# Kernel optimization log

Measured on AMD Instinct MI355X. Metric: run time of the kernel, lower is better.

The kernel has to match this reference:

```python
import jax, jax.numpy as jnp
import numpy as np

HEADS = 16


def setup_inputs() -> dict:
    key = jax.random.key(0)
    ks = jax.random.split(key, 7)
    b, n, dim = 4, 1024, 1024
    s = 1.0 / np.sqrt(dim)
    return {
        "x": jax.random.normal(ks[0], (b, n, dim), dtype=jnp.float32),
        "Wq": jax.random.normal(ks[1], (dim, dim), dtype=jnp.float32) * s,
        "bq": jax.random.normal(ks[2], (dim,), dtype=jnp.float32) * 0.01,
        "Wv": jax.random.normal(ks[3], (dim, dim), dtype=jnp.float32) * s,
        "bv": jax.random.normal(ks[4], (dim,), dtype=jnp.float32) * 0.01,
        "Wo": jax.random.normal(ks[5], (dim, dim), dtype=jnp.float32) * s,
        "bo": jax.random.normal(ks[6], (dim,), dtype=jnp.float32) * 0.01,
    }


def reference(x, Wq, bq, Wv, bv, Wo, bo):
    b, n, dim = x.shape
    h = HEADS
    d = dim // h
    scale = d ** -0.5

    # projections (torch Linear: x @ W.T + b), split heads: b n (h d) -> b h n d
    q = (x @ Wq.T + bq).reshape(b, n, h, d).transpose(0, 2, 1, 3)
    v = (x @ Wv.T + bv).reshape(b, n, h, d).transpose(0, 2, 1, 3)

    # pairwise L2 distance scores: ||q_i||^2 - 2 q_i.q_j + ||q_j||^2
    dots = jnp.einsum("bhnd,bhmd->bhnm", q, q)          # [b,h,n,n]
    sq = jnp.sum(q * q, axis=-1)                          # [b,h,n]
    scores = -(sq[..., :, None] - 2.0 * dots + sq[..., None, :]) * scale
    attn = jax.nn.softmax(scores, axis=-1)

    out = jnp.einsum("bhnm,bhmd->bhnd", attn, v)          # [b,h,n,d]
    out = out.transpose(0, 2, 1, 3).reshape(b, n, dim)    # b h n d -> b n (h d)
    return out @ Wo.T + bo
```

## Files before the change

kernel.cpp:

```cpp
#include <hip/hip_runtime.h>
#include <hip/hip_bf16.h>

typedef __hip_bfloat16 bf16;
typedef short short8 __attribute__((ext_vector_type(8)));
typedef float floatx4 __attribute__((ext_vector_type(4)));
typedef unsigned uintx4 __attribute__((ext_vector_type(4)));
typedef unsigned short ushort;

#define MFMA __builtin_amdgcn_mfma_f32_16x16x32_bf16

#define BATCH 4
#define SEQ   1024
#define DIM   1024
#define HEADS 16
#define HD    64
#define RS    72


__device__ __forceinline__ float b2f(ushort u) {
    union { unsigned i; float f; } x; x.i = (unsigned)u << 16; return x.f;
}
__device__ __forceinline__ ushort f2b(float f) {
    union { float f; unsigned i; } x; x.f = f;
    return (ushort)((x.i + 0x7FFFu + ((x.i >> 16) & 1u)) >> 16);
}

__device__ __forceinline__ void nts16(void* p, uint4 v) {
    uintx4 x; x.x = v.x; x.y = v.y; x.z = v.z; x.w = v.w;
    __builtin_nontemporal_store(x, (uintx4*)p);
}
__device__ __forceinline__ void nts16f(void* p, float4 v) {
    floatx4 x; x.x = v.x; x.y = v.y; x.z = v.z; x.w = v.w;
    __builtin_nontemporal_store(x, (floatx4*)p);
}
__device__ __forceinline__ void nts2(ushort* p, ushort v) {
    __builtin_nontemporal_store(v, p);
}

__device__ __forceinline__ void gload16(const ushort* gp, ushort* lp) {
    __builtin_amdgcn_global_load_lds(
        (const __attribute__((address_space(1))) unsigned*)gp,
        (__attribute__((address_space(3))) unsigned*)lp, 16, 0, 0);
}

__device__ __forceinline__ short8 cvt8(uint4 a, uint4 b) {
    const float* f0 = (const float*)&a;
    const float* f1 = (const float*)&b;
    union { __hip_bfloat162 h; unsigned u; } c0, c1, c2, c3;
    float2 p;
    p.x = f0[0]; p.y = f0[1]; c0.h = __float22bfloat162_rn(p);
    p.x = f0[2]; p.y = f0[3]; c1.h = __float22bfloat162_rn(p);
    p.x = f1[0]; p.y = f1[1]; c2.h = __float22bfloat162_rn(p);
    p.x = f1[2]; p.y = f1[3]; c3.h = __float22bfloat162_rn(p);
    short8 s;
    unsigned* su = (unsigned*)&s;
    su[0] = c0.u; su[1] = c1.u; su[2] = c2.u; su[3] = c3.u;
    return s;
}

__global__ __launch_bounds__(256)
void conv_x(const float* __restrict__ x, ushort* __restrict__ xb)
{
    const size_t g = (size_t)blockIdx.x * 256 + threadIdx.x;
    const uint4* xv = (const uint4*)x;
    uint4 a = xv[g * 2], b = xv[g * 2 + 1];
    short8 s = cvt8(a, b);
    nts16(xb + g * 8, *(uint4*)&s);
}

template<int OUT>
__global__ __launch_bounds__(256, 3)
void gemm_core(const ushort* __restrict__ Ab,
               const float* __restrict__ W0, const float* __restrict__ b0,
               const float* __restrict__ W1, const float* __restrict__ b1,
               ushort* __restrict__ Qd, ushort* __restrict__ Vd,
               float* __restrict__ Fd)
{
    __shared__ __align__(16) ushort SMEM[2 * 128 * 64 + 64 * RS];
    ushort* A0  = SMEM;
    ushort* A1  = SMEM + 8192;
    ushort* Bsm = SMEM + 16384;

    const int t = threadIdx.x;
    const int w = t >> 6, lane = t & 63;
    const int lr = lane & 15, quad = lane >> 4;
    const int isV = (!OUT) && (blockIdx.x >= 16);
    const int n0 = (blockIdx.x & 15) * 64;
    const int m0 = blockIdx.y * 128;
    const float* __restrict__ W    = isV ? W1 : W0;
    const float* __restrict__ bias = isV ? b1 : b0;
    const int mw = (w >> 1) * 64, nw = (w & 1) * 32;
    const int ar = t >> 3, ac8 = (t & 7) * 8;

    const int arow = (lane >> 3);
    const int acS  = ((lane & 7) ^ arow) * 8;

    uint4 wpre[4];
    #pragma unroll
    for (int c = 0; c < 2; ++c) {
        const float* wp = W + (size_t)(n0 + c * 32 + ar) * DIM + ac8;
        wpre[2 * c]     = *(const uint4*)wp;
        wpre[2 * c + 1] = *(const uint4*)(wp + 4);
    }
    {
        #pragma unroll
        for (int i = 0; i < 4; ++i) {
            const int chunk = w * 4 + i;
            const int row = chunk * 8 + arow;
            gload16(Ab + (size_t)(m0 + row) * DIM + acS,
                    A0 + chunk * 512);
        }
    }

    floatx4 acc[4][2];
    const floatx4 fz = {0.f, 0.f, 0.f, 0.f};
    #pragma unroll
    for (int i = 0; i < 4; ++i)
        #pragma unroll
        for (int j = 0; j < 2; ++j) acc[i][j] = fz;

    ushort* Acur = A0;
    ushort* Anxt = A1;

    for (int kt = 0; kt < 16; ++kt) {
        #pragma unroll
        for (int c = 0; c < 2; ++c)
            *(short8*)&Bsm[(c * 32 + ar) * RS + ac8] = cvt8(wpre[2 * c], wpre[2 * c + 1]);
        __syncthreads();
        if (kt < 15) {
            const int k0 = (kt + 1) * 64;
            #pragma unroll
            for (int i = 0; i < 4; ++i) {
                const int chunk = w * 4 + i;
                const int row = chunk * 8 + arow;
                gload16(Ab + (size_t)(m0 + row) * DIM + k0 + acS,
                        Anxt + chunk * 512);
            }
            #pragma unroll
            for (int c = 0; c < 2; ++c) {
                const float* wp = W + (size_t)(n0 + c * 32 + ar) * DIM + k0 + ac8;
                wpre[2 * c]     = *(const uint4*)wp;
                wpre[2 * c + 1] = *(const uint4*)(wp + 4);
            }
        }
        #pragma unroll
        for (int ks = 0; ks < 2; ++ks) {
            short8 af[4], bfx[2];
            #pragma unroll
            for (int tm = 0; tm < 4; ++tm) {
                const int rowa = mw + tm * 16 + lr;
                const int csw  = ((ks * 4 + quad) ^ (lr & 7)) * 8;
                af[tm] = *(const short8*)&Acur[rowa * 64 + csw];
            }
            #pragma unroll
            for (int tn = 0; tn < 2; ++tn)
                bfx[tn] = *(const short8*)&Bsm[(nw + tn * 16 + lr) * RS + ks * 32 + quad * 8];
            #pragma unroll
            for (int tm = 0; tm < 4; ++tm)
                #pragma unroll
                for (int tn = 0; tn < 2; ++tn)
                    acc[tm][tn] = MFMA(af[tm], bfx[tn], acc[tm][tn], 0, 0, 0);
        }
        __syncthreads();
        ushort* tmp = Acur; Acur = Anxt; Anxt = tmp;
    }

    if (OUT) {
        float* TF = (float*)SMEM;
        #pragma unroll
        for (int pass = 0; pass < 2; ++pass) {
            __syncthreads();
            if ((w >> 1) == pass) {
                #pragma unroll
                for (int tn = 0; tn < 2; ++tn) {
                    const float bval = bias[n0 + nw + tn * 16 + lr];
                    #pragma unroll
                    for (int tm = 0; tm < 4; ++tm)
                        #pragma unroll
                        for (int r = 0; r < 4; ++r)
                            TF[(tm * 16 + quad * 4 + r) * 68 + nw + tn * 16 + lr] =
                                acc[tm][tn][r] + bval;
                }
            }
            __syncthreads();
            #pragma unroll
            for (int it = 0; it < 4; ++it) {
                const int cid = it * 256 + t;
                const int row = cid >> 4, c4 = (cid & 15) * 4;
                nts16f(Fd + (size_t)(m0 + pass * 64 + row) * DIM + n0 + c4,
                       *(const float4*)&TF[row * 68 + c4]);
            }
        }
        return;
    }

    const int bb = m0 >> 10, ii0 = m0 & 1023;
    const int head = blockIdx.x & 15;
    const int bh = bb * HEADS + head;
    if (!isV) {
        #pragma unroll
        for (int tn = 0; tn < 2; ++tn) {
            const float bval = bias[n0 + nw + tn * 16 + lr];
            #pragma unroll
            for (int tm = 0; tm < 4; ++tm)
                #pragma unroll
                for (int r = 0; r < 4; ++r)
                    SMEM[(mw + tm * 16 + quad * 4 + r) * 80 + nw + tn * 16 + lr] =
                        f2b(acc[tm][tn][r] + bval);
        }
        __syncthreads();
        #pragma unroll
        for (int it = 0; it < 4; ++it) {
            const int cid = it * 256 + t;
            const int row = cid >> 3, col8 = (cid & 7) * 8;
            nts16(Qd + ((size_t)bh * SEQ + ii0 + row) * HD + col8,
                  *(const uint4*)&SMEM[row * 80 + col8]);
        }
    } else {
        #pragma unroll
        for (int tn = 0; tn < 2; ++tn) {
            const float bval = bias[n0 + nw + tn * 16 + lr];
            #pragma unroll
            for (int tm = 0; tm < 4; ++tm)
                #pragma unroll
                for (int r = 0; r < 4; ++r)
                    SMEM[(nw + tn * 16 + lr) * 144 + mw + tm * 16 + quad * 4 + r] =
                        f2b(acc[tm][tn][r] + bval);
        }
        __syncthreads();
        #pragma unroll
        for (int it = 0; it < 4; ++it) {
            const int cid = it * 256 + t;
            const int row = cid >> 4, col8 = (cid & 15) * 8;
            nts16(Vd + ((size_t)bh * HD + row) * SEQ + ii0 + col8,
                  *(const uint4*)&SMEM[row * 144 + col8]);
        }
    }
}

__global__ __launch_bounds__(256)
void attn_mfma(const ushort* __restrict__ Q, const ushort* __restrict__ Vt,
               ushort* __restrict__ O)
{
    __shared__ __align__(16) ushort Ps[128 * RS];
    __shared__ __align__(16) ushort Ks[64 * RS];
    __shared__ __align__(16) ushort Vs[64 * RS];
    __shared__ float sqq[128], sqk[64];

    const int t = threadIdx.x;
    const int w = t >> 6, lane = t & 63;
    const int lr = lane & 15, quad = lane >> 4;
    const int id = blockIdx.x;
    const int bh = id & 63;
    const int i0 = (id >> 6) * 128;
    const ushort* __restrict__ Qp = Q  + (size_t)bh * SEQ * HD;
    const ushort* __restrict__ Vp = Vt + (size_t)bh * HD * SEQ;

    const int sr = t >> 3, sc8 = (t & 7) * 8;

    #pragma unroll
    for (int it = 0; it < 4; ++it) {
        const int cid = it * 256 + t;
        const int r = cid >> 3, c8 = (cid & 7) * 8;
        *(uint4*)&Ps[r * RS + c8] = *(const uint4*)(Qp + (size_t)(i0 + r) * HD + c8);
    }
    __syncthreads();

    {
        const int qsub = quad & 1, half = quad >> 1;
        const int qr = w * 32 + qsub * 16 + lr, ch = half * 32;
        float s = 0.f;
        #pragma unroll
        for (int cc = 0; cc < 4; ++cc) {
            uint4 k = *(const uint4*)&Ps[qr * RS + ch + cc * 8];
            const ushort* u = (const ushort*)&k;
            #pragma unroll
            for (int e = 0; e < 8; ++e) { float f = b2f(u[e]); s += f * f; }
        }
        s += __shfl_xor(s, 32);
        if (half == 0) sqq[qr] = s;
    }
    __syncthreads();

    short8 qa[2][2];
    #pragma unroll
    for (int tm = 0; tm < 2; ++tm)
        #pragma unroll
        for (int ks = 0; ks < 2; ++ks)
            qa[tm][ks] = *(const short8*)&Ps[(w * 32 + tm * 16 + lr) * RS + ks * 32 + quad * 8];
    float sqi[2][4];
    #pragma unroll
    for (int tm = 0; tm < 2; ++tm)
        #pragma unroll
        for (int r = 0; r < 4; ++r)
            sqi[tm][r] = sqq[w * 32 + tm * 16 + quad * 4 + r];

    floatx4 oacc[2][4];
    const floatx4 fz = {0.f, 0.f, 0.f, 0.f};
    float lrow[2][4] = {};
    #pragma unroll
    for (int tm = 0; tm < 2; ++tm)
        #pragma unroll
        for (int td = 0; td < 4; ++td) oacc[tm][td] = fz;

    for (int jt = 0; jt < 16; ++jt) {
        const int j0 = jt * 64;
        __syncthreads();
        #pragma unroll
        for (int it = 0; it < 2; ++it) {
            const int r = it * 32 + sr;
            *(uint4*)&Ks[r * RS + sc8] = *(const uint4*)(Qp + (size_t)(j0 + r) * HD + sc8);
            *(uint4*)&Vs[r * RS + sc8] = *(const uint4*)(Vp + (size_t)r * SEQ + j0 + sc8);
        }
        __syncthreads();

        {
            const int jr = w * 16 + lr, ch = quad * 16;
            uint4 k1 = *(const uint4*)&Ks[jr * RS + ch];
            uint4 k2 = *(const uint4*)&Ks[jr * RS + ch + 8];
            const ushort* u1 = (const ushort*)&k1;
            const ushort* u2 = (const ushort*)&k2;
            float s = 0.f;
            #pragma unroll
            for (int cc = 0; cc < 8; ++cc) {
                float f1 = b2f(u1[cc]), f2 = b2f(u2[cc]);
                s += f1 * f1 + f2 * f2;
            }
            s += __shfl_xor(s, 16);
            s += __shfl_xor(s, 32);
            if (quad == 0) sqk[jr] = s;
        }
        __syncthreads();

        float sq4[4];
        #pragma unroll
        for (int tn = 0; tn < 4; ++tn) sq4[tn] = sqk[tn * 16 + lr];

        short8 kb[4][2];
        #pragma unroll
        for (int tn = 0; tn < 4; ++tn)
            #pragma unroll
            for (int ks = 0; ks < 2; ++ks)
                kb[tn][ks] = *(const short8*)&Ks[(tn * 16 + lr) * RS + ks * 32 + quad * 8];

        #pragma unroll
        for (int tm = 0; tm < 2; ++tm) {
            floatx4 sacc[4];
            #pragma unroll
            for (int tn = 0; tn < 4; ++tn) {
                floatx4 a = MFMA(qa[tm][0], kb[tn][0], fz, 0, 0, 0);
                sacc[tn]  = MFMA(qa[tm][1], kb[tn][1], a, 0, 0, 0);
            }
            float sc[4][4];
            #pragma unroll
            for (int tn = 0; tn < 4; ++tn) {
                const float msq = -0.125f * sq4[tn];
                #pragma unroll
                for (int r = 0; r < 4; ++r)
                    sc[tn][r] = __expf(0.25f * sacc[tn][r] + msq - 0.125f * sqi[tm][r]);
            }
            #pragma unroll
            for (int r = 0; r < 4; ++r)
                lrow[tm][r] += sc[0][r] + sc[1][r] + sc[2][r] + sc[3][r];
            #pragma unroll
            for (int tp = 0; tp < 2; ++tp)
                #pragma unroll
                for (int r = 0; r < 4; ++r) {
                    float2 fp; fp.x = sc[2 * tp][r]; fp.y = sc[2 * tp + 1][r];
                    union { __hip_bfloat162 h; unsigned u; } cv;
                    cv.h = __float22bfloat162_rn(fp);
                    const int rowb = (w * 32 + tm * 16 + quad * 4 + r) * RS + lr;
                    Ps[rowb + (2 * tp) * 16]     = (ushort)(cv.u & 0xffffu);
                    Ps[rowb + (2 * tp + 1) * 16] = (ushort)(cv.u >> 16);
                }
        }
        __syncthreads();

        short8 pa[2][2], vb[4][2];
        #pragma unroll
        for (int tm = 0; tm < 2; ++tm)
            #pragma unroll
            for (int ks = 0; ks < 2; ++ks)
                pa[tm][ks] = *(const short8*)&Ps[(w * 32 + tm * 16 + lr) * RS + ks * 32 + quad * 8];
        #pragma unroll
        for (int td = 0; td < 4; ++td)
            #pragma unroll
            for (int ks = 0; ks < 2; ++ks)
                vb[td][ks] = *(const short8*)&Vs[(td * 16 + lr) * RS + ks * 32 + quad * 8];
        #pragma unroll
        for (int tm = 0; tm < 2; ++tm)
            #pragma unroll
            for (int td = 0; td < 4; ++td) {
                oacc[tm][td] = MFMA(pa[tm][0], vb[td][0], oacc[tm][td], 0, 0, 0);
                oacc[tm][td] = MFMA(pa[tm][1], vb[td][1], oacc[tm][td], 0, 0, 0);
            }
    }

    const int bb = bh >> 4, head = bh & 15;
    #pragma unroll
    for (int tm = 0; tm < 2; ++tm)
        #pragma unroll
        for (int r = 0; r < 4; ++r) {
            float l = lrow[tm][r];
            l += __shfl_xor(l, 1);
            l += __shfl_xor(l, 2);
            l += __shfl_xor(l, 4);
            l += __shfl_xor(l, 8);
            const float inv = 1.f / l;
            const int row = i0 + w * 32 + tm * 16 + quad * 4 + r;
            #pragma unroll
            for (int td = 0; td < 4; ++td) {
                nts2(O + (size_t)(bb * SEQ + row) * DIM + head * HD + td * 16 + lr,
                     f2b(oacc[tm][td][r] * inv));
            }
        }
}

extern "C" void kernel_launch(void* const* d_in, const int* in_sizes, int n_in,
                              void* d_out, int out_size, void* d_ws, size_t ws_size,
                              hipStream_t stream)
{
    const float* x  = (const float*)d_in[0];
    const float* Wq = (const float*)d_in[1];
    const float* bq = (const float*)d_in[2];
    const float* Wv = (const float*)d_in[3];
    const float* bv = (const float*)d_in[4];
    const float* Wo = (const float*)d_in[5];
    const float* bo = (const float*)d_in[6];

    ushort* Qh = (ushort*)d_ws;
    ushort* Vt = Qh + (size_t)BATCH * HEADS * SEQ * HD;
    ushort* R  = Vt + (size_t)BATCH * HEADS * SEQ * HD;

    conv_x<<<2048, 256, 0, stream>>>(x, R);
    gemm_core<0><<<dim3(32, 32), 256, 0, stream>>>(R, Wq, bq, Wv, bv, Qh, Vt, nullptr);
    attn_mfma<<<512, 256, 0, stream>>>(Qh, Vt, R);
    gemm_core<1><<<dim3(16, 32), 256, 0, stream>>>(R, Wo, bo, nullptr, nullptr,
                                                   nullptr, nullptr, (float*)d_out);
}
```

Before: 183.8 us.

## Double-buffer K/V and W tiles, precompute squared Q norms in projection epilogue

The projection GEMM now double-buffers the converted weight tile, which removes one barrier per k-step. The attention kernel loads K/V tiles asynchronously into double-buffered, XOR-swizzled shared memory and drops the per-tile squared-norm reduction and its two barriers. Squared row norms of Q are instead computed once in the Q-projection epilogue and written to a global buffer. If the workspace is too small, that buffer falls back to d_out, which gets overwritten later, and the attention kernel now requests an occupancy of 3 blocks.

```diff
diff --git a/kernel.cpp b/kernel.cpp
--- a/kernel.cpp
+++ b/kernel.cpp
@@ -74,13 +74,9 @@
                const float* __restrict__ W0, const float* __restrict__ b0,
                const float* __restrict__ W1, const float* __restrict__ b1,
                ushort* __restrict__ Qd, ushort* __restrict__ Vd,
-               float* __restrict__ Fd)
+               float* __restrict__ Fd, float* __restrict__ sqQ)
 {
-    __shared__ __align__(16) ushort SMEM[2 * 128 * 64 + 64 * RS];
-    ushort* A0  = SMEM;
-    ushort* A1  = SMEM + 8192;
-    ushort* Bsm = SMEM + 16384;
-
+    __shared__ __align__(16) ushort SMEM[2 * 8192 + 2 * 64 * RS];
     const int t = threadIdx.x;
     const int w = t >> 6, lane = t & 63;
     const int lr = lane & 15, quad = lane >> 4;
@@ -91,9 +87,13 @@
     const float* __restrict__ bias = isV ? b1 : b0;
     const int mw = (w >> 1) * 64, nw = (w & 1) * 32;
     const int ar = t >> 3, ac8 = (t & 7) * 8;
-
-    const int arow = (lane >> 3);
+    const int arow = lane >> 3;
     const int acS  = ((lane & 7) ^ arow) * 8;
+
+    ushort* Acur = SMEM;
+    ushort* Anxt = SMEM + 8192;
+    ushort* Bcur = SMEM + 16384;
+    ushort* Bnxt = SMEM + 16384 + 64 * RS;
 
     uint4 wpre[4];
     #pragma unroll
@@ -102,15 +102,16 @@
         wpre[2 * c]     = *(const uint4*)wp;
         wpre[2 * c + 1] = *(const uint4*)(wp + 4);
     }
-    {
-        #pragma unroll
-        for (int i = 0; i < 4; ++i) {
-            const int chunk = w * 4 + i;
-            const int row = chunk * 8 + arow;
-            gload16(Ab + (size_t)(m0 + row) * DIM + acS,
-                    A0 + chunk * 512);
-        }
-    }
+    #pragma unroll
+    for (int i = 0; i < 4; ++i) {
+        const int chunk = w * 4 + i;
+        gload16(Ab + (size_t)(m0 + chunk * 8 + arow) * DIM + acS,
+                Acur + chunk * 512);
+    }
+    #pragma unroll
+    for (int c = 0; c < 2; ++c)
+        *(short8*)&Bcur[(c * 32 + ar) * RS + ac8] = cvt8(wpre[2 * c], wpre[2 * c + 1]);
+    __syncthreads();
 
     floatx4 acc[4][2];
     const floatx4 fz = {0.f, 0.f, 0.f, 0.f};
@@ -119,21 +120,13 @@
         #pragma unroll
         for (int j = 0; j < 2; ++j) acc[i][j] = fz;
 
-    ushort* Acur = A0;
-    ushort* Anxt = A1;
-
     for (int kt = 0; kt < 16; ++kt) {
-        #pragma unroll
-        for (int c = 0; c < 2; ++c)
-            *(short8*)&Bsm[(c * 32 + ar) * RS + ac8] = cvt8(wpre[2 * c], wpre[2 * c + 1]);
-        __syncthreads();
         if (kt < 15) {
             const int k0 = (kt + 1) * 64;
             #pragma unroll
             for (int i = 0; i < 4; ++i) {
                 const int chunk = w * 4 + i;
-                const int row = chunk * 8 + arow;
-                gload16(Ab + (size_t)(m0 + row) * DIM + k0 + acS,
+                gload16(Ab + (size_t)(m0 + chunk * 8 + arow) * DIM + k0 + acS,
                         Anxt + chunk * 512);
             }
             #pragma unroll
@@ -149,20 +142,27 @@
             #pragma unroll
             for (int tm = 0; tm < 4; ++tm) {
                 const int rowa = mw + tm * 16 + lr;
-                const int csw  = ((ks * 4 + quad) ^ (lr & 7)) * 8;
+                const int csw  = (((ks << 2) | quad) ^ (lr & 7)) * 8;
                 af[tm] = *(const short8*)&Acur[rowa * 64 + csw];
             }
             #pragma unroll
             for (int tn = 0; tn < 2; ++tn)
-                bfx[tn] = *(const short8*)&Bsm[(nw + tn * 16 + lr) * RS + ks * 32 + quad * 8];
+                bfx[tn] = *(const short8*)&Bcur[(nw + tn * 16 + lr) * RS + ks * 32 + quad * 8];
             #pragma unroll
             for (int tm = 0; tm < 4; ++tm)
                 #pragma unroll
                 for (int tn = 0; tn < 2; ++tn)
                     acc[tm][tn] = MFMA(af[tm], bfx[tn], acc[tm][tn], 0, 0, 0);
         }
+        if (kt < 15) {
+            #pragma unroll
+            for (int c = 0; c < 2; ++c)
+                *(short8*)&Bnxt[(c * 32 + ar) * RS + ac8] = cvt8(wpre[2 * c], wpre[2 * c + 1]);
+        }
         __syncthreads();
-        ushort* tmp = Acur; Acur = Anxt; Anxt = tmp;
+        ushort* tp;
+        tp = Acur; Acur = Anxt; Anxt = tp;
+        tp = Bcur; Bcur = Bnxt; Bnxt = tp;
     }
 
     if (OUT) {
@@ -209,6 +209,19 @@
                         f2b(acc[tm][tn][r] + bval);
         }
         __syncthreads();
+        {
+            const int row = t >> 1, half = t & 1;
+            float s = 0.f;
+            #pragma unroll
+            for (int c = 0; c < 4; ++c) {
+                uint4 kk = *(const uint4*)&SMEM[row * 80 + half * 32 + c * 8];
+                const ushort* u = (const ushort*)&kk;
+                #pragma unroll
+                for (int e = 0; e < 8; ++e) { float f = b2f(u[e]); s += f * f; }
+            }
+            s += __shfl_xor(s, 1);
+            if (half == 0) sqQ[(size_t)bh * SEQ + ii0 + row] = s;
+        }
         #pragma unroll
         for (int it = 0; it < 4; ++it) {
             const int cid = it * 256 + t;
@@ -238,14 +251,12 @@
     }
 }
 
-__global__ __launch_bounds__(256)
+__global__ __launch_bounds__(256, 3)
 void attn_mfma(const ushort* __restrict__ Q, const ushort* __restrict__ Vt,
-               ushort* __restrict__ O)
+               const float* __restrict__ sqG, ushort* __restrict__ O)
 {
     __shared__ __align__(16) ushort Ps[128 * RS];
-    __shared__ __align__(16) ushort Ks[64 * RS];
-    __shared__ __align__(16) ushort Vs[64 * RS];
-    __shared__ float sqq[128], sqk[64];
+    __shared__ __align__(16) ushort KV[4 * 4096];
 
     const int t = threadIdx.x;
     const int w = t >> 6, lane = t & 63;
@@ -255,9 +266,22 @@
     const int i0 = (id >> 6) * 128;
     const ushort* __restrict__ Qp = Q  + (size_t)bh * SEQ * HD;
     const ushort* __restrict__ Vp = Vt + (size_t)bh * HD * SEQ;
-
-    const int sr = t >> 3, sc8 = (t & 7) * 8;
-
+    const float*  __restrict__ sqB = sqG + (size_t)bh * SEQ;
+
+    const int arow = lane >> 3;
+    const int acS  = ((lane & 7) ^ arow) * 8;
+
+    ushort* Kcur = KV;
+    ushort* Vcur = KV + 4096;
+    ushort* Knxt = KV + 8192;
+    ushort* Vnxt = KV + 12288;
+
+    #pragma unroll
+    for (int i = 0; i < 2; ++i) {
+        const int c = w + i * 4;
+        gload16(Qp + (size_t)(c * 8 + arow) * HD + acS, Kcur + c * 512);
+        gload16(Vp + (size_t)(c * 8 + arow) * SEQ + acS, Vcur + c * 512);
+    }
     #pragma unroll
     for (int it = 0; it < 4; ++it) {
         const int cid = it * 256 + t;
@@ -266,22 +290,6 @@
     }
     __syncthreads();
 
-    {
-        const int qsub = quad & 1, half = quad >> 1;
-        const int qr = w * 32 + qsub * 16 + lr, ch = half * 32;
-        float s = 0.f;
-        #pragma unroll
-        for (int cc = 0; cc < 4; ++cc) {
-            uint4 k = *(const uint4*)&Ps[qr * RS + ch + cc * 8];
-            const ushort* u = (const ushort*)&k;
-            #pragma unroll
-            for (int e = 0; e < 8; ++e) { float f = b2f(u[e]); s += f * f; }
-        }
-        s += __shfl_xor(s, 32);
-        if (half == 0) sqq[qr] = s;
-    }
-    __syncthreads();
-
     short8 qa[2][2];
     #pragma unroll
     for (int tm = 0; tm < 2; ++tm)
@@ -293,7 +301,7 @@
     for (int tm = 0; tm < 2; ++tm)
         #pragma unroll
         for (int r = 0; r < 4; ++r)
-            sqi[tm][r] = sqq[w * 32 + tm * 16 + quad * 4 + r];
+            sqi[tm][r] = sqB[i0 + w * 32 + tm * 16 + quad * 4 + r];
 
     floatx4 oacc[2][4];
     const floatx4 fz = {0.f, 0.f, 0.f, 0.f};
@@ -304,44 +312,27 @@
         for (int td = 0; td < 4; ++td) oacc[tm][td] = fz;
 
     for (int jt = 0; jt < 16; ++jt) {
-        const int j0 = jt * 64;
-        __syncthreads();
-        #pragma unroll
-        for (int it = 0; it < 2; ++it) {
-            const int r = it * 32 + sr;
-            *(uint4*)&Ks[r * RS + sc8] = *(const uint4*)(Qp + (size_t)(j0 + r) * HD + sc8);
-            *(uint4*)&Vs[r * RS + sc8] = *(const uint4*)(Vp + (size_t)r * SEQ + j0 + sc8);
-        }
-        __syncthreads();
-
-        {
-            const int jr = w * 16 + lr, ch = quad * 16;
-            uint4 k1 = *(const uint4*)&Ks[jr * RS + ch];
-            uint4 k2 = *(const uint4*)&Ks[jr * RS + ch + 8];
-            const ushort* u1 = (const ushort*)&k1;
-            const ushort* u2 = (const ushort*)&k2;
-            float s = 0.f;
-            #pragma unroll
-            for (int cc = 0; cc < 8; ++cc) {
-                float f1 = b2f(u1[cc]), f2 = b2f(u2[cc]);
-                s += f1 * f1 + f2 * f2;
-            }
-            s += __shfl_xor(s, 16);
-            s += __shfl_xor(s, 32);
-            if (quad == 0) sqk[jr] = s;
-        }
-        __syncthreads();
-
+        if (jt < 15) {
+            const int j0n = (jt + 1) * 64;
+            #pragma unroll
+            for (int i = 0; i < 2; ++i) {
+                const int c = w + i * 4;
+                gload16(Qp + (size_t)(j0n + c * 8 + arow) * HD + acS, Knxt + c * 512);
+                gload16(Vp + (size_t)(c * 8 + arow) * SEQ + j0n + acS, Vnxt + c * 512);
+            }
+        }
         float sq4[4];
         #pragma unroll
-        for (int tn = 0; tn < 4; ++tn) sq4[tn] = sqk[tn * 16 + lr];
+        for (int tn = 0; tn < 4; ++tn) sq4[tn] = sqB[jt * 64 + tn * 16 + lr];
 
         short8 kb[4][2];
         #pragma unroll
         for (int tn = 0; tn < 4; ++tn)
             #pragma unroll
-            for (int ks = 0; ks < 2; ++ks)
-                kb[tn][ks] = *(const short8*)&Ks[(tn * 16 + lr) * RS + ks * 32 + quad * 8];
+            for (int ks = 0; ks < 2; ++ks) {
+                const int row = tn * 16 + lr;
+                kb[tn][ks] = *(const short8*)&Kcur[row * 64 + ((((ks << 2) | quad)) ^ (lr & 7)) * 8];
+            }
 
         #pragma unroll
         for (int tm = 0; tm < 2; ++tm) {
@@ -374,8 +365,6 @@
                     Ps[rowb + (2 * tp + 1) * 16] = (ushort)(cv.u >> 16);
                 }
         }
-        __syncthreads();
-
         short8 pa[2][2], vb[4][2];
         #pragma unroll
         for (int tm = 0; tm < 2; ++tm)
@@ -385,8 +374,10 @@
         #pragma unroll
         for (int td = 0; td < 4; ++td)
             #pragma unroll
-            for (int ks = 0; ks < 2; ++ks)
-                vb[td][ks] = *(const short8*)&Vs[(td * 16 + lr) * RS + ks * 32 + quad * 8];
+            for (int ks = 0; ks < 2; ++ks) {
+                const int row = td * 16 + lr;
+                vb[td][ks] = *(const short8*)&Vcur[row * 64 + ((((ks << 2) | quad)) ^ (lr & 7)) * 8];
+            }
         #pragma unroll
         for (int tm = 0; tm < 2; ++tm)
             #pragma unroll
@@ -394,6 +385,10 @@
                 oacc[tm][td] = MFMA(pa[tm][0], vb[td][0], oacc[tm][td], 0, 0, 0);
                 oacc[tm][td] = MFMA(pa[tm][1], vb[td][1], oacc[tm][td], 0, 0, 0);
             }
+        __syncthreads();
+        ushort* tp2;
+        tp2 = Kcur; Kcur = Knxt; Knxt = tp2;
+        tp2 = Vcur; Vcur = Vnxt; Vnxt = tp2;
     }
 
     const int bb = bh >> 4, head = bh & 15;
@@ -431,10 +426,16 @@
     ushort* Qh = (ushort*)d_ws;
     ushort* Vt = Qh + (size_t)BATCH * HEADS * SEQ * HD;
     ushort* R  = Vt + (size_t)BATCH * HEADS * SEQ * HD;
+    const size_t WS3 = (size_t)3 * BATCH * HEADS * SEQ * HD * 2;
+    const size_t SQB = (size_t)BATCH * HEADS * SEQ * 4;
+    float* sqG = (ws_size >= WS3 + SQB) ? (float*)((char*)d_ws + WS3)
+                                        : (float*)d_out;
 
     conv_x<<<2048, 256, 0, stream>>>(x, R);
-    gemm_core<0><<<dim3(32, 32), 256, 0, stream>>>(R, Wq, bq, Wv, bv, Qh, Vt, nullptr);
-    attn_mfma<<<512, 256, 0, stream>>>(Qh, Vt, R);
+    gemm_core<0><<<dim3(32, 32), 256, 0, stream>>>(R, Wq, bq, Wv, bv, Qh, Vt,
+                                                   nullptr, sqG);
+    attn_mfma<<<512, 256, 0, stream>>>(Qh, Vt, sqG, R);
     gemm_core<1><<<dim3(16, 32), 256, 0, stream>>>(R, Wo, bo, nullptr, nullptr,
-                                                   nullptr, nullptr, (float*)d_out);
-}
+                                                   nullptr, nullptr,
+                                                   (float*)d_out, nullptr);
+}
```

After: 186.5 us. About the same (+1.5%).
